# Performance work log

Hardware: AMD Instinct MI355X
Metric: run time of the kernel (lower is better)

## Reference

```python
import jax, jax.numpy as jnp
import numpy as np

WS = 16      # window size
NH = 8       # num heads
LN_EPS = 1e-5
F_NORM_EPS = 1e-12  # torch F.normalize eps


def layer_norm(x, w, b):
    mu = jnp.mean(x, axis=-1, keepdims=True)
    var = jnp.mean((x - mu) ** 2, axis=-1, keepdims=True)
    return (x - mu) / jnp.sqrt(var + LN_EPS) * w + b


def setup_inputs() -> dict:
    key = jax.random.key(0)
    ks = jax.random.split(key, 8)
    b, h, w, c = 2, 192, 192, 128
    n = WS * WS
    x = jax.random.normal(ks[0], (b, h * w, c), dtype=jnp.float32)
    rpi = jax.random.randint(ks[1], (n, n), 0, (2 * WS - 1) ** 2)
    s = 0.02
    inp = {
        'x': x,
        'qkv_w': jax.random.normal(ks[2], (c, 3 * c), jnp.float32) * s,
        'qkv_b': jnp.zeros((3 * c,), jnp.float32),
        'proj_w': jax.random.normal(ks[3], (c, c), jnp.float32) * s,
        'proj_b': jnp.zeros((c,), jnp.float32),
        'logit_scale': jnp.full((NH, 1, 1), jnp.log(10.0), jnp.float32),
        'rpb_table': jax.random.normal(ks[4], ((2 * WS - 1) ** 2, NH), jnp.float32) * s,
        'norm1_w': jnp.ones((c,), jnp.float32),
        'norm1_b': jnp.zeros((c,), jnp.float32),
        'norm2_w': jnp.ones((c,), jnp.float32),
        'norm2_b': jnp.zeros((c,), jnp.float32),
        'fc1_w': jax.random.normal(ks[5], (c, 2 * c), jnp.float32) * s,
        'fc1_b': jnp.zeros((2 * c,), jnp.float32),
        'fc2_w': jax.random.normal(ks[6], (2 * c, c), jnp.float32) * s,
        'fc2_b': jnp.zeros((c,), jnp.float32),
        'h': h,
        'w': w,
        'rpi': rpi,
    }
    return inp


def reference(x, qkv_w, qkv_b, proj_w, proj_b, logit_scale, rpb_table,
              norm1_w, norm1_b, norm2_w, norm2_b, fc1_w, fc1_b, fc2_w, fc2_b,
              h, w, rpi):
    b, L, c = x.shape
    ws, nh = WS, NH
    d = c // nh
    n = ws * ws
    shortcut = x

    # window partition: (b, h, w, c) -> (b*nW, ws*ws, c)
    xi = x.reshape(b, h // ws, ws, w // ws, ws, c)
    xw = xi.transpose(0, 1, 3, 2, 4, 5).reshape(-1, n, c)

    # cosine window attention (SwinV2 style)
    qkv = (xw @ qkv_w + qkv_b).reshape(-1, n, 3, nh, d).transpose(2, 0, 3, 1, 4)
    q, k, v = qkv[0], qkv[1], qkv[2]                       # (B_, nh, n, d)
    qn = q / jnp.maximum(jnp.linalg.norm(q, axis=-1, keepdims=True), F_NORM_EPS)
    kn = k / jnp.maximum(jnp.linalg.norm(k, axis=-1, keepdims=True), F_NORM_EPS)
    scale = jnp.exp(jnp.minimum(logit_scale, jnp.log(100.0)))  # (nh,1,1)
    attn = jnp.einsum('bhnd,bhmd->bhnm', qn, kn) * scale
    bias = rpb_table[rpi.reshape(-1)].reshape(n, n, nh).transpose(2, 0, 1)
    attn = jax.nn.softmax(attn + bias[None], axis=-1)
    out = jnp.einsum('bhnm,bhmd->bhnd', attn, v)
    out = out.transpose(0, 2, 1, 3).reshape(-1, n, c) @ proj_w + proj_b

    # window reverse
    xr = out.reshape(b, h // ws, w // ws, ws, ws, c)
    xr = xr.transpose(0, 1, 3, 2, 4, 5).reshape(b, L, c)

    # res-post-norm residual + MLP (GELU), eval mode (no dropout/drop_path)
    x1 = shortcut + layer_norm(xr, norm1_w, norm1_b)
    y = jax.nn.gelu(x1 @ fc1_w + fc1_b, approximate=False) @ fc2_w + fc2_b
    return x1 + layer_norm(y, norm2_w, norm2_b)
```

## Files before the change

kernel.cpp:

```cpp
#include <hip/hip_runtime.h>
#include <hip/hip_bf16.h>
#include <math.h>

#define BB 2
#define HH 192
#define WW 192
#define CC 128
#define LL (HH*WW)
#define WSZ 16
#define NTOK 256
#define NHEAD 8
#define DHEAD 16
#define NWS 12
#define NWB 144
#define NWT 288
#define MT (BB*LL)

#define OFF_BIAS   0
#define OFF_QKV    262144
#define OFF_ATTN   14417920
#define OFF_X1     19136512
#define OFF_X1B    28573696
#define OFF_HID    33292288
#define OFF_WT     42729472
#define WT_QKV 0
#define WT_PROJ 49152
#define WT_FC1 65536
#define WT_FC2 98304

typedef short  bf16x8 __attribute__((ext_vector_type(8)));
typedef float  f32x4  __attribute__((ext_vector_type(4)));
#define MFMA16(a,b,c) __builtin_amdgcn_mfma_f32_16x16x32_bf16(a,b,c,0,0,0)

__device__ __forceinline__ ushort f2b(float f) {
    uint u = __float_as_uint(f);
    uint r = u + 0x7fffu + ((u >> 16) & 1u);
    return (ushort)(r >> 16);
}
__device__ __forceinline__ float b2f(ushort u) {
    return __uint_as_float(((uint)u) << 16);
}

__device__ __forceinline__ int win_to_g(int wi, int t) {
    int b   = wi / NWB;
    int win = wi - b*NWB;
    int hi  = win / NWS;
    int wj  = win - hi*NWS;
    return b*LL + (hi*WSZ + (t >> 4))*WW + wj*WSZ + (t & 15);
}

__global__ __launch_bounds__(256) void bias_kernel(const int* __restrict__ rpi,
                                                   const float* __restrict__ rpb,
                                                   ushort* __restrict__ biasT) {
    int gid = blockIdx.x*256 + threadIdx.x;
    int j = gid >> 8, i = gid & 255;
    int idx = rpi[i*256 + j];
    #pragma unroll
    for (int h = 0; h < 8; ++h)
        biasT[h*65536 + j*256 + i] = f2b(rpb[idx*8 + h]);
}

__global__ __launch_bounds__(256) void wconv_kernel(const float* __restrict__ qkv_w,
                                                    const float* __restrict__ proj_w,
                                                    const float* __restrict__ fc1_w,
                                                    const float* __restrict__ fc2_w,
                                                    ushort* __restrict__ wt) {
    int gid = blockIdx.x*256 + threadIdx.x;
    if (gid < 49152) {
        int n = gid >> 7, k = gid & 127;
        wt[gid] = f2b(qkv_w[k*384 + n]);
    } else if (gid < 65536) {
        int i = gid - 49152; int n = i >> 7, k = i & 127;
        wt[gid] = f2b(proj_w[k*128 + n]);
    } else if (gid < 98304) {
        int i = gid - 65536; int n = i >> 7, k = i & 127;
        wt[gid] = f2b(fc1_w[k*256 + n]);
    } else {
        int i = gid - 98304; int n = i >> 8, k = i & 255;
        wt[gid] = f2b(fc2_w[k*128 + n]);
    }
}

__global__ __launch_bounds__(256) void qkv_mfma(const float* __restrict__ x,
                                                const ushort* __restrict__ wt,
                                                const float* __restrict__ wb,
                                                const float* __restrict__ lscale,
                                                ushort* __restrict__ qkvbuf) {
    __shared__ ushort alds[64][136];
    const int tid = threadIdx.x;
    const int bx = blockIdx.x;
    const int wi = bx >> 2;
    const int t0w = (bx & 3) << 6;
    #pragma unroll
    for (int it = 0; it < 8; ++it) {
        int idx = it*256 + tid;
        int row = idx >> 5, c4 = idx & 31;
        int g = win_to_g(wi, t0w + row);
        float4 v = ((const float4*)x)[g*32 + c4];
        ushort4 b;
        b.x = f2b(v.x); b.y = f2b(v.y); b.z = f2b(v.z); b.w = f2b(v.w);
        *(ushort4*)&alds[row][c4*4] = b;
    }
    __syncthreads();
    const int wv = tid >> 6, lane = tid & 63;
    const int lr = lane & 15, kg = lane >> 4;
    f32x4 acc[24];
    #pragma unroll
    for (int t = 0; t < 24; ++t) acc[t] = (f32x4)0.f;
    #pragma unroll
    for (int ks = 0; ks < 4; ++ks) {
        bf16x8 af = *(const bf16x8*)&alds[wv*16 + lr][ks*32 + kg*8];
        #pragma unroll
        for (int t = 0; t < 24; ++t) {
            bf16x8 bfr = *(const bf16x8*)(wt + (t*16 + lr)*128 + ks*32 + kg*8);
            acc[t] = MFMA16(af, bfr, acc[t]);
        }
    }
    #pragma unroll
    for (int t = 0; t < 24; ++t) {
        const int s = t >> 3, head = t & 7;
        const float bcol = wb[s*128 + head*16 + lr];
        #pragma unroll
        for (int r = 0; r < 4; ++r) acc[t][r] += bcol;
        if (s < 2) {
            float sc = (s == 0) ? __expf(fminf(lscale[head], 4.6051701860f)) : 1.f;
            #pragma unroll
            for (int r = 0; r < 4; ++r) {
                float ss = acc[t][r]*acc[t][r];
                ss += __shfl_xor(ss, 1);
                ss += __shfl_xor(ss, 2);
                ss += __shfl_xor(ss, 4);
                ss += __shfl_xor(ss, 8);
                acc[t][r] *= sc / fmaxf(sqrtf(ss), 1e-12f);
            }
        }
        ushort* dst = qkvbuf + ((wi*8+head)*3 + s)*4096;
        #pragma unroll
        for (int r = 0; r < 4; ++r) {
            int row = t0w + wv*16 + kg*4 + r;
            dst[row*16 + lr] = f2b(acc[t][r]);
        }
    }
}

__global__ __launch_bounds__(256) void attn_mfma(const ushort* __restrict__ qkv,
                                                 const ushort* __restrict__ biasT,
                                                 ushort* __restrict__ attn_o) {
    __shared__ ushort Vt[16][256];
    __shared__ ushort Plds[4][64][72];
    const int tid = threadIdx.x;
    const int wi = blockIdx.x >> 3, head = blockIdx.x & 7;
    const ushort* qb = qkv + ((wi*8 + head)*3)*4096;
    const ushort* kb = qb + 4096;
    const ushort* vb = qb + 8192;

    {
        const ushort* vr = vb + tid*16;
        #pragma unroll
        for (int c = 0; c < 4; ++c) {
            ushort4 vv = *(const ushort4*)(vr + c*4);
            Vt[c*4+0][tid] = vv.x; Vt[c*4+1][tid] = vv.y;
            Vt[c*4+2][tid] = vv.z; Vt[c*4+3][tid] = vv.w;
        }
    }
    const int wv = tid >> 6, lane = tid & 63;
    const int lr = lane & 15, kg = lane >> 4;

    bf16x8 qf[4];
    #pragma unroll
    for (int mt = 0; mt < 4; ++mt)
        qf[mt] = (kg < 2) ? *(const bf16x8*)(qb + (wv*64 + mt*16 + lr)*16 + kg*8)
                          : (bf16x8)0;
    __syncthreads();

    f32x4 oacc[4];
    #pragma unroll
    for (int mt = 0; mt < 4; ++mt) oacc[mt] = (f32x4)0.f;
    float lsum[4][4];
    #pragma unroll
    for (int mt = 0; mt < 4; ++mt)
        #pragma unroll
        for (int r = 0; r < 4; ++r) lsum[mt][r] = 0.f;

    for (int jt = 0; jt < 4; ++jt) {
        bf16x8 kf[4];
        #pragma unroll
        for (int nt = 0; nt < 4; ++nt)
            kf[nt] = (kg < 2) ? *(const bf16x8*)(kb + (jt*64 + nt*16 + lr)*16 + kg*8)
                              : (bf16x8)0;
        #pragma unroll
        for (int nt = 0; nt < 4; ++nt) {
            f32x4 s[4];
            #pragma unroll
            for (int mt = 0; mt < 4; ++mt)
                s[mt] = MFMA16(qf[mt], kf[nt], (f32x4)0.f);
            const int key = jt*64 + nt*16 + lr;
            #pragma unroll
            for (int mt = 0; mt < 4; ++mt) {
                ushort4 bb = *(const ushort4*)(biasT + head*65536 + key*256
                                               + wv*64 + mt*16 + kg*4);
                float p0 = __expf(s[mt][0] + b2f(bb.x));
                float p1 = __expf(s[mt][1] + b2f(bb.y));
                float p2 = __expf(s[mt][2] + b2f(bb.z));
                float p3 = __expf(s[mt][3] + b2f(bb.w));
                lsum[mt][0] += p0; lsum[mt][1] += p1;
                lsum[mt][2] += p2; lsum[mt][3] += p3;
                Plds[wv][mt*16 + kg*4 + 0][nt*16 + lr] = f2b(p0);
                Plds[wv][mt*16 + kg*4 + 1][nt*16 + lr] = f2b(p1);
                Plds[wv][mt*16 + kg*4 + 2][nt*16 + lr] = f2b(p2);
                Plds[wv][mt*16 + kg*4 + 3][nt*16 + lr] = f2b(p3);
            }
        }
        #pragma unroll
        for (int kt = 0; kt < 2; ++kt) {
            bf16x8 vf = *(const bf16x8*)&Vt[lr][jt*64 + kt*32 + kg*8];
            #pragma unroll
            for (int mt = 0; mt < 4; ++mt) {
                bf16x8 pf = *(const bf16x8*)&Plds[wv][mt*16 + lr][kt*32 + kg*8];
                oacc[mt] = MFMA16(pf, vf, oacc[mt]);
            }
        }
    }
    #pragma unroll
    for (int mt = 0; mt < 4; ++mt) {
        #pragma unroll
        for (int r = 0; r < 4; ++r) {
            float v = lsum[mt][r];
            v += __shfl_xor(v, 1);
            v += __shfl_xor(v, 2);
            v += __shfl_xor(v, 4);
            v += __shfl_xor(v, 8);
            lsum[mt][r] = 1.f / v;
        }
    }
    #pragma unroll
    for (int mt = 0; mt < 4; ++mt) {
        #pragma unroll
        for (int r = 0; r < 4; ++r) {
            int q = wv*64 + mt*16 + kg*4 + r;
            attn_o[(wi*256 + q)*128 + head*16 + lr] = f2b(oacc[mt][r] * lsum[mt][r]);
        }
    }
}

__global__ __launch_bounds__(256) void proj_mfma(const ushort* __restrict__ a,
                                                 const ushort* __restrict__ wt,
                                                 const float* __restrict__ wb,
                                                 const float* __restrict__ x,
                                                 const float* __restrict__ n1w,
                                                 const float* __restrict__ n1b,
                                                 float* __restrict__ x1,
                                                 ushort* __restrict__ x1b) {
    __shared__ ushort alds[64][136];
    const int tid = threadIdx.x;
    const int M0 = blockIdx.x * 64;
    #pragma unroll
    for (int it = 0; it < 8; ++it) {
        int idx = it*256 + tid;
        int row = idx >> 5, c4 = idx & 31;
        *(ushort4*)&alds[row][c4*4] = ((const ushort4*)a)[M0*32 + idx];
    }
    __syncthreads();
    const int wv = tid >> 6, lane = tid & 63;
    const int lr = lane & 15, kg = lane >> 4;
    f32x4 acc[8];
    #pragma unroll
    for (int t = 0; t < 8; ++t) acc[t] = (f32x4)0.f;
    #pragma unroll
    for (int ks = 0; ks < 4; ++ks) {
        bf16x8 af = *(const bf16x8*)&alds[wv*16 + lr][ks*32 + kg*8];
        #pragma unroll
        for (int t = 0; t < 8; ++t) {
            bf16x8 bfr = *(const bf16x8*)(wt + (t*16 + lr)*128 + ks*32 + kg*8);
            acc[t] = MFMA16(af, bfr, acc[t]);
        }
    }
    #pragma unroll
    for (int t = 0; t < 8; ++t) {
        float bcol = wb[t*16 + lr];
        #pragma unroll
        for (int r = 0; r < 4; ++r) acc[t][r] += bcol;
    }
    float mu_[4], rs_[4];
    #pragma unroll
    for (int r = 0; r < 4; ++r) {
        float s = 0.f, q = 0.f;
        #pragma unroll
        for (int t = 0; t < 8; ++t) { float v = acc[t][r]; s += v; q += v*v; }
        s += __shfl_xor(s,1); q += __shfl_xor(q,1);
        s += __shfl_xor(s,2); q += __shfl_xor(q,2);
        s += __shfl_xor(s,4); q += __shfl_xor(q,4);
        s += __shfl_xor(s,8); q += __shfl_xor(q,8);
        float mu = s*(1.f/128.f);
        float var = q*(1.f/128.f) - mu*mu;
        mu_[r] = mu; rs_[r] = rsqrtf(var + 1e-5f);
    }
    float w1c[8], b1c[8];
    #pragma unroll
    for (int t = 0; t < 8; ++t) { w1c[t] = n1w[t*16+lr]; b1c[t] = n1b[t*16+lr]; }
    #pragma unroll
    for (int r = 0; r < 4; ++r) {
        int M = M0 + wv*16 + kg*4 + r;
        int g = win_to_g(M >> 8, M & 255);
        #pragma unroll
        for (int t = 0; t < 8; ++t) {
            int col = t*16 + lr;
            float val = x[g*128 + col] + (acc[t][r]-mu_[r])*rs_[r]*w1c[t] + b1c[t];
            x1[g*128 + col] = val;
            x1b[g*128 + col] = f2b(val);
        }
    }
}

__global__ __launch_bounds__(256) void fc1_mfma(const ushort* __restrict__ a,
                                                const ushort* __restrict__ wt,
                                                const float* __restrict__ wb,
                                                ushort* __restrict__ hidden) {
    __shared__ ushort alds[64][136];
    const int tid = threadIdx.x;
    const int M0 = blockIdx.x * 64;
    #pragma unroll
    for (int it = 0; it < 8; ++it) {
        int idx = it*256 + tid;
        int row = idx >> 5, c4 = idx & 31;
        *(ushort4*)&alds[row][c4*4] = ((const ushort4*)a)[M0*32 + idx];
    }
    __syncthreads();
    const int wv = tid >> 6, lane = tid & 63;
    const int lr = lane & 15, kg = lane >> 4;
    f32x4 acc[16];
    #pragma unroll
    for (int t = 0; t < 16; ++t) acc[t] = (f32x4)0.f;
    #pragma unroll
    for (int ks = 0; ks < 4; ++ks) {
        bf16x8 af = *(const bf16x8*)&alds[wv*16 + lr][ks*32 + kg*8];
        #pragma unroll
        for (int t = 0; t < 16; ++t) {
            bf16x8 bfr = *(const bf16x8*)(wt + (t*16 + lr)*128 + ks*32 + kg*8);
            acc[t] = MFMA16(af, bfr, acc[t]);
        }
    }
    #pragma unroll
    for (int t = 0; t < 16; ++t) {
        float bcol = wb[t*16 + lr];
        int col = t*16 + lr;
        #pragma unroll
        for (int r = 0; r < 4; ++r) {
            int row = M0 + wv*16 + kg*4 + r;
            float v = acc[t][r] + bcol;
            float gl = v*0.5f*(1.f + erff(v*0.70710678118654752f));
            hidden[row*256 + col] = f2b(gl);
        }
    }
}

__global__ __launch_bounds__(256) void fc2_mfma(const ushort* __restrict__ a,
                                                const ushort* __restrict__ wt,
                                                const float* __restrict__ wb,
                                                const float* __restrict__ x1,
                                                const float* __restrict__ n2w,
                                                const float* __restrict__ n2b,
                                                float* __restrict__ out) {
    __shared__ ushort alds[64][264];
    const int tid = threadIdx.x;
    const int M0 = blockIdx.x * 64;
    #pragma unroll
    for (int it = 0; it < 16; ++it) {
        int idx = it*256 + tid;
        int row = idx >> 6, c4 = idx & 63;
        *(ushort4*)&alds[row][c4*4] = ((const ushort4*)a)[M0*64 + idx];
    }
    __syncthreads();
    const int wv = tid >> 6, lane = tid & 63;
    const int lr = lane & 15, kg = lane >> 4;
    f32x4 acc[8];
    #pragma unroll
    for (int t = 0; t < 8; ++t) acc[t] = (f32x4)0.f;
    #pragma unroll
    for (int ks = 0; ks < 8; ++ks) {
        bf16x8 af = *(const bf16x8*)&alds[wv*16 + lr][ks*32 + kg*8];
        #pragma unroll
        for (int t = 0; t < 8; ++t) {
            bf16x8 bfr = *(const bf16x8*)(wt + (t*16 + lr)*256 + ks*32 + kg*8);
            acc[t] = MFMA16(af, bfr, acc[t]);
        }
    }
    #pragma unroll
    for (int t = 0; t < 8; ++t) {
        float bcol = wb[t*16 + lr];
        #pragma unroll
        for (int r = 0; r < 4; ++r) acc[t][r] += bcol;
    }
    float mu_[4], rs_[4];
    #pragma unroll
    for (int r = 0; r < 4; ++r) {
        float s = 0.f, q = 0.f;
        #pragma unroll
        for (int t = 0; t < 8; ++t) { float v = acc[t][r]; s += v; q += v*v; }
        s += __shfl_xor(s,1); q += __shfl_xor(q,1);
        s += __shfl_xor(s,2); q += __shfl_xor(q,2);
        s += __shfl_xor(s,4); q += __shfl_xor(q,4);
        s += __shfl_xor(s,8); q += __shfl_xor(q,8);
        float mu = s*(1.f/128.f);
        float var = q*(1.f/128.f) - mu*mu;
        mu_[r] = mu; rs_[r] = rsqrtf(var + 1e-5f);
    }
    float w2c[8], b2c[8];
    #pragma unroll
    for (int t = 0; t < 8; ++t) { w2c[t] = n2w[t*16+lr]; b2c[t] = n2b[t*16+lr]; }
    #pragma unroll
    for (int r = 0; r < 4; ++r) {
        int g = M0 + wv*16 + kg*4 + r;
        #pragma unroll
        for (int t = 0; t < 8; ++t) {
            int col = t*16 + lr;
            out[g*128 + col] = x1[g*128 + col] + (acc[t][r]-mu_[r])*rs_[r]*w2c[t] + b2c[t];
        }
    }
}

extern "C" void kernel_launch(void* const* d_in, const int* in_sizes, int n_in,
                              void* d_out, int out_size, void* d_ws, size_t ws_size,
                              hipStream_t stream) {
    const float* x      = (const float*)d_in[0];
    const float* qkv_w  = (const float*)d_in[1];
    const float* qkv_b  = (const float*)d_in[2];
    const float* proj_w = (const float*)d_in[3];
    const float* proj_b = (const float*)d_in[4];
    const float* lscale = (const float*)d_in[5];
    const float* rpb    = (const float*)d_in[6];
    const float* n1w    = (const float*)d_in[7];
    const float* n1b    = (const float*)d_in[8];
    const float* n2w    = (const float*)d_in[9];
    const float* n2b    = (const float*)d_in[10];
    const float* fc1_w  = (const float*)d_in[11];
    const float* fc1_b  = (const float*)d_in[12];
    const float* fc2_w  = (const float*)d_in[13];
    const float* fc2_b  = (const float*)d_in[14];
    const int*   rpi    = (const int*)d_in[17];
    float* out = (float*)d_out;

    float* ws      = (float*)d_ws;
    ushort* biasT  = (ushort*)(ws + OFF_BIAS);
    ushort* qkvbuf = (ushort*)(ws + OFF_QKV);
    ushort* attn_o = (ushort*)(ws + OFF_ATTN);
    float*  x1     = ws + OFF_X1;
    ushort* x1b    = (ushort*)(ws + OFF_X1B);
    ushort* hidden = (ushort*)(ws + OFF_HID);
    ushort* wt     = (ushort*)(ws + OFF_WT);

    bias_kernel<<<256, 256, 0, stream>>>(rpi, rpb, biasT);
    wconv_kernel<<<512, 256, 0, stream>>>(qkv_w, proj_w, fc1_w, fc2_w, wt);
    qkv_mfma<<<1152, 256, 0, stream>>>(x, wt + WT_QKV, qkv_b, lscale, qkvbuf);
    attn_mfma<<<2304, 256, 0, stream>>>(qkvbuf, biasT, attn_o);
    proj_mfma<<<1152, 256, 0, stream>>>(attn_o, wt + WT_PROJ, proj_b, x, n1w, n1b, x1, x1b);
    fc1_mfma<<<1152, 256, 0, stream>>>(x1b, wt + WT_FC1, fc1_b, hidden);
    fc2_mfma<<<1152, 256, 0, stream>>>(hidden, wt + WT_FC2, fc2_b, x1, n2w, n2b, out);
}
```

Before: 424.0 us.

## Double M-tile per block in GEMM kernels to reuse weight fragments

The qkv, proj, fc1 and fc2 GEMM kernels now handle 128 rows per block instead of 64, with each wave computing two 16-row M tiles. Each weight fragment loaded from global memory is reused across both tiles, and the loops are reordered so weights are loaded per output tile. In qkv and fc1, accumulators are now per N-tile, which lowers register pressure. fc2 splits its K dimension into two LDS stages to keep shared memory at 128x136. Grids are halved to 576 blocks, which reduces parallelism and latency hiding across the CUs.

```diff
diff --git a/kernel.cpp b/kernel.cpp
--- a/kernel.cpp
+++ b/kernel.cpp
@@ -86,13 +86,12 @@
                                                 const float* __restrict__ wb,
                                                 const float* __restrict__ lscale,
                                                 ushort* __restrict__ qkvbuf) {
-    __shared__ ushort alds[64][136];
+    __shared__ ushort alds[128][136];
     const int tid = threadIdx.x;
-    const int bx = blockIdx.x;
-    const int wi = bx >> 2;
-    const int t0w = (bx & 3) << 6;
-    #pragma unroll
-    for (int it = 0; it < 8; ++it) {
+    const int wi  = blockIdx.x >> 1;
+    const int t0w = (blockIdx.x & 1) << 7;
+    #pragma unroll
+    for (int it = 0; it < 16; ++it) {
         int idx = it*256 + tid;
         int row = idx >> 5, c4 = idx & 31;
         int g = win_to_g(wi, t0w + row);
@@ -104,42 +103,55 @@
     __syncthreads();
     const int wv = tid >> 6, lane = tid & 63;
     const int lr = lane & 15, kg = lane >> 4;
-    f32x4 acc[24];
-    #pragma unroll
-    for (int t = 0; t < 24; ++t) acc[t] = (f32x4)0.f;
-    #pragma unroll
-    for (int ks = 0; ks < 4; ++ks) {
-        bf16x8 af = *(const bf16x8*)&alds[wv*16 + lr][ks*32 + kg*8];
-        #pragma unroll
-        for (int t = 0; t < 24; ++t) {
-            bf16x8 bfr = *(const bf16x8*)(wt + (t*16 + lr)*128 + ks*32 + kg*8);
-            acc[t] = MFMA16(af, bfr, acc[t]);
-        }
-    }
-    #pragma unroll
+    bf16x8 af[2][4];
+    #pragma unroll
+    for (int mt = 0; mt < 2; ++mt)
+        #pragma unroll
+        for (int ks = 0; ks < 4; ++ks)
+            af[mt][ks] = *(const bf16x8*)&alds[wv*32 + mt*16 + lr][ks*32 + kg*8];
+
+    #pragma unroll 4
     for (int t = 0; t < 24; ++t) {
+        bf16x8 bfr[4];
+        #pragma unroll
+        for (int ks = 0; ks < 4; ++ks)
+            bfr[ks] = *(const bf16x8*)(wt + (t*16 + lr)*128 + ks*32 + kg*8);
+        f32x4 acc[2];
+        acc[0] = (f32x4)0.f; acc[1] = (f32x4)0.f;
+        #pragma unroll
+        for (int mt = 0; mt < 2; ++mt)
+            #pragma unroll
+            for (int ks = 0; ks < 4; ++ks)
+                acc[mt] = MFMA16(af[mt][ks], bfr[ks], acc[mt]);
+
         const int s = t >> 3, head = t & 7;
         const float bcol = wb[s*128 + head*16 + lr];
         #pragma unroll
-        for (int r = 0; r < 4; ++r) acc[t][r] += bcol;
+        for (int mt = 0; mt < 2; ++mt)
+            #pragma unroll
+            for (int r = 0; r < 4; ++r) acc[mt][r] += bcol;
         if (s < 2) {
             float sc = (s == 0) ? __expf(fminf(lscale[head], 4.6051701860f)) : 1.f;
             #pragma unroll
+            for (int mt = 0; mt < 2; ++mt)
+                #pragma unroll
+                for (int r = 0; r < 4; ++r) {
+                    float ss = acc[mt][r]*acc[mt][r];
+                    ss += __shfl_xor(ss, 1);
+                    ss += __shfl_xor(ss, 2);
+                    ss += __shfl_xor(ss, 4);
+                    ss += __shfl_xor(ss, 8);
+                    acc[mt][r] *= sc / fmaxf(sqrtf(ss), 1e-12f);
+                }
+        }
+        ushort* dst = qkvbuf + ((wi*8+head)*3 + s)*4096;
+        #pragma unroll
+        for (int mt = 0; mt < 2; ++mt)
+            #pragma unroll
             for (int r = 0; r < 4; ++r) {
-                float ss = acc[t][r]*acc[t][r];
-                ss += __shfl_xor(ss, 1);
-                ss += __shfl_xor(ss, 2);
-                ss += __shfl_xor(ss, 4);
-                ss += __shfl_xor(ss, 8);
-                acc[t][r] *= sc / fmaxf(sqrtf(ss), 1e-12f);
+                int row = t0w + wv*32 + mt*16 + kg*4 + r;
+                dst[row*16 + lr] = f2b(acc[mt][r]);
             }
-        }
-        ushort* dst = qkvbuf + ((wi*8+head)*3 + s)*4096;
-        #pragma unroll
-        for (int r = 0; r < 4; ++r) {
-            int row = t0w + wv*16 + kg*4 + r;
-            dst[row*16 + lr] = f2b(acc[t][r]);
-        }
     }
 }
 
@@ -153,7 +165,6 @@
     const ushort* qb = qkv + ((wi*8 + head)*3)*4096;
     const ushort* kb = qb + 4096;
     const ushort* vb = qb + 8192;
-
     {
         const ushort* vr = vb + tid*16;
         #pragma unroll
@@ -165,7 +176,6 @@
     }
     const int wv = tid >> 6, lane = tid & 63;
     const int lr = lane & 15, kg = lane >> 4;
-
     bf16x8 qf[4];
     #pragma unroll
     for (int mt = 0; mt < 4; ++mt)
@@ -251,11 +261,11 @@
                                                  const float* __restrict__ n1b,
                                                  float* __restrict__ x1,
                                                  ushort* __restrict__ x1b) {
-    __shared__ ushort alds[64][136];
+    __shared__ ushort alds[128][136];
     const int tid = threadIdx.x;
-    const int M0 = blockIdx.x * 64;
-    #pragma unroll
-    for (int it = 0; it < 8; ++it) {
+    const int M0 = blockIdx.x * 128;
+    #pragma unroll
+    for (int it = 0; it < 16; ++it) {
         int idx = it*256 + tid;
         int row = idx >> 5, c4 = idx & 31;
         *(ushort4*)&alds[row][c4*4] = ((const ushort4*)a)[M0*32 + idx];
@@ -263,64 +273,83 @@
     __syncthreads();
     const int wv = tid >> 6, lane = tid & 63;
     const int lr = lane & 15, kg = lane >> 4;
-    f32x4 acc[8];
-    #pragma unroll
-    for (int t = 0; t < 8; ++t) acc[t] = (f32x4)0.f;
-    #pragma unroll
-    for (int ks = 0; ks < 4; ++ks) {
-        bf16x8 af = *(const bf16x8*)&alds[wv*16 + lr][ks*32 + kg*8];
-        #pragma unroll
-        for (int t = 0; t < 8; ++t) {
-            bf16x8 bfr = *(const bf16x8*)(wt + (t*16 + lr)*128 + ks*32 + kg*8);
-            acc[t] = MFMA16(af, bfr, acc[t]);
-        }
+    bf16x8 af[2][4];
+    #pragma unroll
+    for (int mt = 0; mt < 2; ++mt)
+        #pragma unroll
+        for (int ks = 0; ks < 4; ++ks)
+            af[mt][ks] = *(const bf16x8*)&alds[wv*32 + mt*16 + lr][ks*32 + kg*8];
+
+    f32x4 acc[2][8];
+    #pragma unroll
+    for (int mt = 0; mt < 2; ++mt)
+        #pragma unroll
+        for (int t = 0; t < 8; ++t) acc[mt][t] = (f32x4)0.f;
+    #pragma unroll
+    for (int t = 0; t < 8; ++t) {
+        bf16x8 bfr[4];
+        #pragma unroll
+        for (int ks = 0; ks < 4; ++ks)
+            bfr[ks] = *(const bf16x8*)(wt + (t*16 + lr)*128 + ks*32 + kg*8);
+        #pragma unroll
+        for (int mt = 0; mt < 2; ++mt)
+            #pragma unroll
+            for (int ks = 0; ks < 4; ++ks)
+                acc[mt][t] = MFMA16(af[mt][ks], bfr[ks], acc[mt][t]);
     }
     #pragma unroll
     for (int t = 0; t < 8; ++t) {
         float bcol = wb[t*16 + lr];
         #pragma unroll
-        for (int r = 0; r < 4; ++r) acc[t][r] += bcol;
-    }
-    float mu_[4], rs_[4];
-    #pragma unroll
-    for (int r = 0; r < 4; ++r) {
-        float s = 0.f, q = 0.f;
-        #pragma unroll
-        for (int t = 0; t < 8; ++t) { float v = acc[t][r]; s += v; q += v*v; }
-        s += __shfl_xor(s,1); q += __shfl_xor(q,1);
-        s += __shfl_xor(s,2); q += __shfl_xor(q,2);
-        s += __shfl_xor(s,4); q += __shfl_xor(q,4);
-        s += __shfl_xor(s,8); q += __shfl_xor(q,8);
-        float mu = s*(1.f/128.f);
-        float var = q*(1.f/128.f) - mu*mu;
-        mu_[r] = mu; rs_[r] = rsqrtf(var + 1e-5f);
-    }
+        for (int mt = 0; mt < 2; ++mt)
+            #pragma unroll
+            for (int r = 0; r < 4; ++r) acc[mt][t][r] += bcol;
+    }
+    float mu_[2][4], rs_[2][4];
+    #pragma unroll
+    for (int mt = 0; mt < 2; ++mt)
+        #pragma unroll
+        for (int r = 0; r < 4; ++r) {
+            float s = 0.f, q = 0.f;
+            #pragma unroll
+            for (int t = 0; t < 8; ++t) { float v = acc[mt][t][r]; s += v; q += v*v; }
+            s += __shfl_xor(s,1); q += __shfl_xor(q,1);
+            s += __shfl_xor(s,2); q += __shfl_xor(q,2);
+            s += __shfl_xor(s,4); q += __shfl_xor(q,4);
+            s += __shfl_xor(s,8); q += __shfl_xor(q,8);
+            float mu = s*(1.f/128.f);
+            float var = q*(1.f/128.f) - mu*mu;
+            mu_[mt][r] = mu; rs_[mt][r] = rsqrtf(var + 1e-5f);
+        }
     float w1c[8], b1c[8];
     #pragma unroll
     for (int t = 0; t < 8; ++t) { w1c[t] = n1w[t*16+lr]; b1c[t] = n1b[t*16+lr]; }
     #pragma unroll
-    for (int r = 0; r < 4; ++r) {
-        int M = M0 + wv*16 + kg*4 + r;
-        int g = win_to_g(M >> 8, M & 255);
-        #pragma unroll
-        for (int t = 0; t < 8; ++t) {
-            int col = t*16 + lr;
-            float val = x[g*128 + col] + (acc[t][r]-mu_[r])*rs_[r]*w1c[t] + b1c[t];
-            x1[g*128 + col] = val;
-            x1b[g*128 + col] = f2b(val);
-        }
-    }
+    for (int mt = 0; mt < 2; ++mt)
+        #pragma unroll
+        for (int r = 0; r < 4; ++r) {
+            int M = M0 + wv*32 + mt*16 + kg*4 + r;
+            int g = win_to_g(M >> 8, M & 255);
+            #pragma unroll
+            for (int t = 0; t < 8; ++t) {
+                int col = t*16 + lr;
+                float val = x[g*128 + col]
+                          + (acc[mt][t][r]-mu_[mt][r])*rs_[mt][r]*w1c[t] + b1c[t];
+                x1[g*128 + col] = val;
+                x1b[g*128 + col] = f2b(val);
+            }
+        }
 }
 
 __global__ __launch_bounds__(256) void fc1_mfma(const ushort* __restrict__ a,
                                                 const ushort* __restrict__ wt,
                                                 const float* __restrict__ wb,
                                                 ushort* __restrict__ hidden) {
-    __shared__ ushort alds[64][136];
+    __shared__ ushort alds[128][136];
     const int tid = threadIdx.x;
-    const int M0 = blockIdx.x * 64;
-    #pragma unroll
-    for (int it = 0; it < 8; ++it) {
+    const int M0 = blockIdx.x * 128;
+    #pragma unroll
+    for (int it = 0; it < 16; ++it) {
         int idx = it*256 + tid;
         int row = idx >> 5, c4 = idx & 31;
         *(ushort4*)&alds[row][c4*4] = ((const ushort4*)a)[M0*32 + idx];
@@ -328,29 +357,37 @@
     __syncthreads();
     const int wv = tid >> 6, lane = tid & 63;
     const int lr = lane & 15, kg = lane >> 4;
-    f32x4 acc[16];
-    #pragma unroll
-    for (int t = 0; t < 16; ++t) acc[t] = (f32x4)0.f;
-    #pragma unroll
-    for (int ks = 0; ks < 4; ++ks) {
-        bf16x8 af = *(const bf16x8*)&alds[wv*16 + lr][ks*32 + kg*8];
-        #pragma unroll
-        for (int t = 0; t < 16; ++t) {
-            bf16x8 bfr = *(const bf16x8*)(wt + (t*16 + lr)*128 + ks*32 + kg*8);
-            acc[t] = MFMA16(af, bfr, acc[t]);
-        }
-    }
-    #pragma unroll
+    bf16x8 af[2][4];
+    #pragma unroll
+    for (int mt = 0; mt < 2; ++mt)
+        #pragma unroll
+        for (int ks = 0; ks < 4; ++ks)
+            af[mt][ks] = *(const bf16x8*)&alds[wv*32 + mt*16 + lr][ks*32 + kg*8];
+
+    #pragma unroll 4
     for (int t = 0; t < 16; ++t) {
+        bf16x8 bfr[4];
+        #pragma unroll
+        for (int ks = 0; ks < 4; ++ks)
+            bfr[ks] = *(const bf16x8*)(wt + (t*16 + lr)*128 + ks*32 + kg*8);
+        f32x4 acc[2];
+        acc[0] = (f32x4)0.f; acc[1] = (f32x4)0.f;
+        #pragma unroll
+        for (int mt = 0; mt < 2; ++mt)
+            #pragma unroll
+            for (int ks = 0; ks < 4; ++ks)
+                acc[mt] = MFMA16(af[mt][ks], bfr[ks], acc[mt]);
         float bcol = wb[t*16 + lr];
         int col = t*16 + lr;
         #pragma unroll
-        for (int r = 0; r < 4; ++r) {
-            int row = M0 + wv*16 + kg*4 + r;
-            float v = acc[t][r] + bcol;
-            float gl = v*0.5f*(1.f + erff(v*0.70710678118654752f));
-            hidden[row*256 + col] = f2b(gl);
-        }
+        for (int mt = 0; mt < 2; ++mt)
+            #pragma unroll
+            for (int r = 0; r < 4; ++r) {
+                int row = M0 + wv*32 + mt*16 + kg*4 + r;
+                float v = acc[mt][r] + bcol;
+                float gl = v*0.5f*(1.f + erff(v*0.70710678118654752f));
+                hidden[row*256 + col] = f2b(gl);
+            }
     }
 }
 
@@ -361,62 +398,85 @@
                                                 const float* __restrict__ n2w,
                                                 const float* __restrict__ n2b,
                                                 float* __restrict__ out) {
-    __shared__ ushort alds[64][264];
+    __shared__ ushort alds[128][136];
     const int tid = threadIdx.x;
-    const int M0 = blockIdx.x * 64;
-    #pragma unroll
-    for (int it = 0; it < 16; ++it) {
-        int idx = it*256 + tid;
-        int row = idx >> 6, c4 = idx & 63;
-        *(ushort4*)&alds[row][c4*4] = ((const ushort4*)a)[M0*64 + idx];
-    }
-    __syncthreads();
+    const int M0 = blockIdx.x * 128;
     const int wv = tid >> 6, lane = tid & 63;
     const int lr = lane & 15, kg = lane >> 4;
-    f32x4 acc[8];
-    #pragma unroll
-    for (int t = 0; t < 8; ++t) acc[t] = (f32x4)0.f;
-    #pragma unroll
-    for (int ks = 0; ks < 8; ++ks) {
-        bf16x8 af = *(const bf16x8*)&alds[wv*16 + lr][ks*32 + kg*8];
+    f32x4 acc[2][8];
+    #pragma unroll
+    for (int mt = 0; mt < 2; ++mt)
+        #pragma unroll
+        for (int t = 0; t < 8; ++t) acc[mt][t] = (f32x4)0.f;
+
+    for (int ko = 0; ko < 2; ++ko) {
+        if (ko) __syncthreads();
+        #pragma unroll
+        for (int it = 0; it < 16; ++it) {
+            int idx = it*256 + tid;
+            int row = idx >> 5, c4 = idx & 31;
+            *(ushort4*)&alds[row][c4*4] =
+                *(const ushort4*)(a + (M0+row)*256 + ko*128 + c4*4);
+        }
+        __syncthreads();
+        bf16x8 af[2][4];
+        #pragma unroll
+        for (int mt = 0; mt < 2; ++mt)
+            #pragma unroll
+            for (int ks = 0; ks < 4; ++ks)
+                af[mt][ks] = *(const bf16x8*)&alds[wv*32 + mt*16 + lr][ks*32 + kg*8];
         #pragma unroll
         for (int t = 0; t < 8; ++t) {
-            bf16x8 bfr = *(const bf16x8*)(wt + (t*16 + lr)*256 + ks*32 + kg*8);
-            acc[t] = MFMA16(af, bfr, acc[t]);
+            bf16x8 bfr[4];
+            #pragma unroll
+            for (int ks = 0; ks < 4; ++ks)
+                bfr[ks] = *(const bf16x8*)(wt + (t*16 + lr)*256 + ko*128 + ks*32 + kg*8);
+            #pragma unroll
+            for (int mt = 0; mt < 2; ++mt)
+                #pragma unroll
+                for (int ks = 0; ks < 4; ++ks)
+                    acc[mt][t] = MFMA16(af[mt][ks], bfr[ks], acc[mt][t]);
         }
     }
     #pragma unroll
     for (int t = 0; t < 8; ++t) {
         float bcol = wb[t*16 + lr];
         #pragma unroll
-        for (int r = 0; r < 4; ++r) acc[t][r] += bcol;
-    }
-    float mu_[4], rs_[4];
-    #pragma unroll
-    for (int r = 0; r < 4; ++r) {
-        float s = 0.f, q = 0.f;
-        #pragma unroll
-        for (int t = 0; t < 8; ++t) { float v = acc[t][r]; s += v; q += v*v; }
-        s += __shfl_xor(s,1); q += __shfl_xor(q,1);
-        s += __shfl_xor(s,2); q += __shfl_xor(q,2);
-        s += __shfl_xor(s,4); q += __shfl_xor(q,4);
-        s += __shfl_xor(s,8); q += __shfl_xor(q,8);
-        float mu = s*(1.f/128.f);
-        float var = q*(1.f/128.f) - mu*mu;
-        mu_[r] = mu; rs_[r] = rsqrtf(var + 1e-5f);
-    }
+        for (int mt = 0; mt < 2; ++mt)
+            #pragma unroll
+            for (int r = 0; r < 4; ++r) acc[mt][t][r] += bcol;
+    }
+    float mu_[2][4], rs_[2][4];
+    #pragma unroll
+    for (int mt = 0; mt < 2; ++mt)
+        #pragma unroll
+        for (int r = 0; r < 4; ++r) {
+            float s = 0.f, q = 0.f;
+            #pragma unroll
+            for (int t = 0; t < 8; ++t) { float v = acc[mt][t][r]; s += v; q += v*v; }
+            s += __shfl_xor(s,1); q += __shfl_xor(q,1);
+            s += __shfl_xor(s,2); q += __shfl_xor(q,2);
+            s += __shfl_xor(s,4); q += __shfl_xor(q,4);
+            s += __shfl_xor(s,8); q += __shfl_xor(q,8);
+            float mu = s*(1.f/128.f);
+            float var = q*(1.f/128.f) - mu*mu;
+            mu_[mt][r] = mu; rs_[mt][r] = rsqrtf(var + 1e-5f);
+        }
     float w2c[8], b2c[8];
     #pragma unroll
     for (int t = 0; t < 8; ++t) { w2c[t] = n2w[t*16+lr]; b2c[t] = n2b[t*16+lr]; }
     #pragma unroll
-    for (int r = 0; r < 4; ++r) {
-        int g = M0 + wv*16 + kg*4 + r;
-        #pragma unroll
-        for (int t = 0; t < 8; ++t) {
-            int col = t*16 + lr;
-            out[g*128 + col] = x1[g*128 + col] + (acc[t][r]-mu_[r])*rs_[r]*w2c[t] + b2c[t];
-        }
-    }
+    for (int mt = 0; mt < 2; ++mt)
+        #pragma unroll
+        for (int r = 0; r < 4; ++r) {
+            int g = M0 + wv*32 + mt*16 + kg*4 + r;
+            #pragma unroll
+            for (int t = 0; t < 8; ++t) {
+                int col = t*16 + lr;
+                out[g*128 + col] = x1[g*128 + col]
+                                 + (acc[mt][t][r]-mu_[mt][r])*rs_[mt][r]*w2c[t] + b2c[t];
+            }
+        }
 }
 
 extern "C" void kernel_launch(void* const* d_in, const int* in_sizes, int n_in,
@@ -451,9 +511,9 @@
 
     bias_kernel<<<256, 256, 0, stream>>>(rpi, rpb, biasT);
     wconv_kernel<<<512, 256, 0, stream>>>(qkv_w, proj_w, fc1_w, fc2_w, wt);
-    qkv_mfma<<<1152, 256, 0, stream>>>(x, wt + WT_QKV, qkv_b, lscale, qkvbuf);
+    qkv_mfma<<<576, 256, 0, stream>>>(x, wt + WT_QKV, qkv_b, lscale, qkvbuf);
     attn_mfma<<<2304, 256, 0, stream>>>(qkvbuf, biasT, attn_o);
-    proj_mfma<<<1152, 256, 0, stream>>>(attn_o, wt + WT_PROJ, proj_b, x, n1w, n1b, x1, x1b);
-    fc1_mfma<<<1152, 256, 0, stream>>>(x1b, wt + WT_FC1, fc1_b, hidden);
-    fc2_mfma<<<1152, 256, 0, stream>>>(hidden, wt + WT_FC2, fc2_b, x1, n2w, n2b, out);
-}
+    proj_mfma<<<576, 256, 0, stream>>>(attn_o, wt + WT_PROJ, proj_b, x, n1w, n1b, x1, x1b);
+    fc1_mfma<<<576, 256, 0, stream>>>(x1b, wt + WT_FC1, fc1_b, hidden);
+    fc2_mfma<<<576, 256, 0, stream>>>(hidden, wt + WT_FC2, fc2_b, x1, n2w, n2b, out);
+}
```

New measurement: 354.7 us. -16.4%, faster.
